# Optimization experiments

Measured on AMD Instinct MI355X. Metric: run time of the kernel, lower is better.

## Reference

```python
import jax, jax.numpy as jnp
import numpy as np
import math

SCALE = 35.0
MARGIN = 0.5
THRESH = -math.cos(MARGIN)          # easy_margin=False branch
SIN_M = math.sin(MARGIN)
OUT_INDICATOR = 1.0                 # easy_margin=False branch

B, D, C = 256, 128, 100000


def setup_inputs() -> dict:
    key = jax.random.key(0)
    k1, k2, k3 = jax.random.split(key, 3)
    feat = jax.random.normal(k1, (B, D), dtype=jnp.float32)
    # xavier_uniform over [class_num, feature_dim]
    limit = math.sqrt(6.0 / (C + D))
    weights = jax.random.uniform(k2, (C, D), dtype=jnp.float32, minval=-limit, maxval=limit)
    label = jax.random.randint(k3, (B,), 0, C, dtype=jnp.int64)
    return {"feat": feat, "weights": weights, "label": label}


def reference(feat, weights, label):
    # cosine similarity between l2-normalized features and class weights
    nf = feat / jnp.linalg.norm(feat, axis=-1, keepdims=True)          # [B, D]
    nw = weights / jnp.linalg.norm(weights, axis=-1, keepdims=True)    # [C, D]
    cos = jnp.einsum('bd,cd->bc', nf, nw)                              # [B, C]
    innerproduct_logits = jnp.einsum('bd,cd->bc', feat, weights)       # [B, C]

    rows = jnp.arange(cos.shape[0])
    cos_gt = cos[rows, label]                                          # [B]

    # margin tables are zero off the ground-truth column, so
    # cos(acos(cos)+0) == cos there: only the gt entry changes.
    cond = cos_gt > THRESH
    add_m = jnp.where(cond, MARGIN, 0.0)
    ext = jnp.where(cond, 0.0, -MARGIN * SIN_M) * OUT_INDICATOR
    # clip for acos numerical safety (matmul of normalized vecs can exceed 1 by eps)
    gt_marg = jnp.cos(jnp.arccos(jnp.clip(cos_gt, -1.0, 1.0)) + add_m) + ext

    marginal_logits = (SCALE * cos).at[rows, label].set(SCALE * gt_marg)
    return (cos, marginal_logits, innerproduct_logits)
```

## Files before the change

### kernel.cpp

```cpp
#include <hip/hip_runtime.h>
#include <math.h>

using short8  = __attribute__((ext_vector_type(8))) short;
using floatx4 = __attribute__((ext_vector_type(4))) float;

namespace {
constexpr int   kB      = 256;
constexpr int   kD      = 128;
constexpr int   kC      = 100000;
constexpr float kScale  = 35.0f;
constexpr float kCosM   = 0.87758256189037276f;
constexpr float kSinM   = 0.47942553860420301f;
constexpr float kThresh = -0.87758256189037276f;
constexpr float kExt    = -0.5f * 0.47942553860420301f;

constexpr size_t kFeatBfOff = 0;
constexpr size_t kRfOff     = (size_t)kB * 256;
}

__device__ inline unsigned short f2bf(float f) {
    unsigned u = __builtin_bit_cast(unsigned, f);
    return (unsigned short)((u + 0x7fffu + ((u >> 16) & 1u)) >> 16);
}

__device__ inline void async16(void* lds, const void* g) {
    __builtin_amdgcn_global_load_lds(
        (const __attribute__((address_space(1))) void*)g,
        (__attribute__((address_space(3))) void*)lds, 16, 0, 0);
}

__global__ __launch_bounds__(256)
void arcface_prep(const float* __restrict__ feat, unsigned char* __restrict__ ws) {
    const int wid = blockIdx.x * 4 + (threadIdx.x >> 6);
    const int l   = threadIdx.x & 63;
    const float2 v = *(const float2*)(feat + (size_t)wid * kD + 2 * l);
    float s = v.x * v.x + v.y * v.y;
    #pragma unroll
    for (int off = 32; off > 0; off >>= 1) s += __shfl_down(s, off, 64);
    const unsigned packed = (unsigned)f2bf(v.x) | ((unsigned)f2bf(v.y) << 16);
    ((unsigned*)(ws + kFeatBfOff + (size_t)wid * 256))[l] = packed;
    if (l == 0) *(float*)(ws + kRfOff + (size_t)wid * 4) = rsqrtf(s);
}

__global__ __launch_bounds__(256, 2)
void arcface_gemm(const float* __restrict__ wgt,
                  const unsigned char* __restrict__ ws,
                  float* __restrict__ out_cos,
                  float* __restrict__ out_marg,
                  float* __restrict__ out_ip) {
    __shared__ float sW[64 * 128];
    __shared__ float sScr[4][16 * 68];
    __shared__ float sRw[64];

    const int t   = threadIdx.x;
    const int l   = t & 63;
    const int w   = t >> 6;
    const int q   = l >> 4;
    const int c16 = l & 15;
    const int m0  = w * 64;
    const int c0  = blockIdx.x * 64;

    #pragma unroll
    for (int p = 0; p < 8; ++p) {
        const int o    = p * 4096 + t * 16;
        const int row  = o >> 9;
        const int col  = o & 511;
        const int swz  = ((row & 15) << 5) | ((row & 4) << 2);
        const int srow = min(c0 + row, kC - 1);
        async16((char*)sW + o, (const char*)wgt + (size_t)srow * 512 + (col ^ swz));
    }

    const short* featbf = (const short*)(ws + kFeatBfOff);
    const float* rf_g   = (const float*)(ws + kRfOff);

    short8 aF[4][4];
    #pragma unroll
    for (int mi = 0; mi < 4; ++mi)
        #pragma unroll
        for (int kq = 0; kq < 4; ++kq)
            aF[mi][kq] = *(const short8*)(featbf + (size_t)(m0 + mi * 16 + c16) * kD + kq * 32 + q * 8);

    __syncthreads();

    floatx4 acc[4][4];
    #pragma unroll
    for (int mi = 0; mi < 4; ++mi)
        #pragma unroll
        for (int nt = 0; nt < 4; ++nt)
            acc[mi][nt] = (floatx4){0.f, 0.f, 0.f, 0.f};

    float s2[4] = {0.f, 0.f, 0.f, 0.f};

    #pragma unroll
    for (int kq = 0; kq < 4; ++kq) {
        short8 bF[4];
        #pragma unroll
        for (int nt = 0; nt < 4; ++nt) {
            const int row = nt * 16 + c16;
            const int swz = ((row & 15) << 5) | ((row & 4) << 2);
            const int cb  = kq * 128 + q * 32;
            const floatx4 w0 = *(const floatx4*)((const char*)sW + row * 512 + ((cb)      ^ swz));
            const floatx4 w1 = *(const floatx4*)((const char*)sW + row * 512 + ((cb + 16) ^ swz));
            s2[nt] += w0[0]*w0[0] + w0[1]*w0[1] + w0[2]*w0[2] + w0[3]*w0[3]
                    + w1[0]*w1[0] + w1[1]*w1[1] + w1[2]*w1[2] + w1[3]*w1[3];
            short8 b;
            b[0] = (short)f2bf(w0[0]); b[1] = (short)f2bf(w0[1]);
            b[2] = (short)f2bf(w0[2]); b[3] = (short)f2bf(w0[3]);
            b[4] = (short)f2bf(w1[0]); b[5] = (short)f2bf(w1[1]);
            b[6] = (short)f2bf(w1[2]); b[7] = (short)f2bf(w1[3]);
            bF[nt] = b;
        }
        #pragma unroll
        for (int mi = 0; mi < 4; ++mi)
            #pragma unroll
            for (int nt = 0; nt < 4; ++nt)
                acc[mi][nt] = __builtin_amdgcn_mfma_f32_16x16x32_bf16(
                    aF[mi][kq], bF[nt], acc[mi][nt], 0, 0, 0);
    }

    #pragma unroll
    for (int nt = 0; nt < 4; ++nt) {
        float s = s2[nt];
        s += __shfl_xor(s, 16, 64);
        s += __shfl_xor(s, 32, 64);
        sRw[nt * 16 + c16] = rsqrtf(s);
    }

    float* scr = &sScr[w][0];
    const int  c   = c0 + c16 * 4;
    const bool cok = c < kC;
    const floatx4 rw4 = *(const floatx4*)(sRw + c16 * 4);

    #pragma unroll
    for (int mi = 0; mi < 4; ++mi) {
        #pragma unroll
        for (int nt = 0; nt < 4; ++nt)
            #pragma unroll
            for (int r = 0; r < 4; ++r)
                scr[(q * 4 + r) * 68 + nt * 16 + c16] = acc[mi][nt][r];
        #pragma unroll
        for (int jj = 0; jj < 4; ++jj) {
            const int rr = q + 4 * jj;
            const floatx4 ip = *(const floatx4*)(scr + rr * 68 + c16 * 4);
            const int m = m0 + mi * 16 + rr;
            if (cok) {
                const float rf = rf_g[m];
                const floatx4 cs = ip * rf * rw4;
                const size_t o = (size_t)m * kC + c;
                __builtin_nontemporal_store(ip,           (floatx4*)(out_ip + o));
                __builtin_nontemporal_store(cs,           (floatx4*)(out_cos + o));
                __builtin_nontemporal_store(cs * kScale,  (floatx4*)(out_marg + o));
            }
        }
    }
}

__global__ void arcface_fixup(const int* __restrict__ label,
                              const float* __restrict__ out_cos,
                              float* __restrict__ out_marg) {
    const int b = threadIdx.x;
    bool is64 = true;
    #pragma unroll
    for (int i = 1; i < 24; i += 2) is64 = is64 && (label[i] == 0);
    const int c = is64 ? label[2 * b] : label[b];
    const size_t idx = (size_t)b * kC + c;
    const float cosv = out_cos[idx];
    const float cc = fminf(1.f, fmaxf(-1.f, cosv));
    float marg;
    if (cosv > kThresh) {
        marg = cc * kCosM - sqrtf(fmaxf(0.f, 1.f - cc * cc)) * kSinM;
    } else {
        marg = cc + kExt;
    }
    out_marg[idx] = kScale * marg;
}

extern "C" void kernel_launch(void* const* d_in, const int* in_sizes, int n_in,
                              void* d_out, int out_size, void* d_ws, size_t ws_size,
                              hipStream_t stream) {
    const float* feat  = (const float*)d_in[0];
    const float* wgt   = (const float*)d_in[1];
    const int*   label = (const int*)d_in[2];
    float* out_cos  = (float*)d_out;
    float* out_marg = out_cos  + (size_t)kB * kC;
    float* out_ip   = out_marg + (size_t)kB * kC;
    unsigned char* ws = (unsigned char*)d_ws;

    arcface_prep<<<64, 256, 0, stream>>>(feat, ws);
    arcface_gemm<<<(kC + 63) / 64, 256, 0, stream>>>(wgt, ws, out_cos, out_marg, out_ip);
    arcface_fixup<<<1, 256, 0, stream>>>(label, out_cos, out_marg);
}
```

Measured before the change: 358.2 us.

## Switch GEMM to persistent per-wave tiles loading weights directly from global

```diff
diff --git a/kernel.cpp b/kernel.cpp
--- a/kernel.cpp
+++ b/kernel.cpp
@@ -16,17 +16,16 @@
 
 constexpr size_t kFeatBfOff = 0;
 constexpr size_t kRfOff     = (size_t)kB * 256;
+
+constexpr int kNgroups   = (kC + 63) / 64;
+constexpr int kTiles     = 8 * kNgroups;
+constexpr int kGemmGrid  = 512;
+constexpr int kWaveSlots = kGemmGrid * 4;
 }
 
 __device__ inline unsigned short f2bf(float f) {
     unsigned u = __builtin_bit_cast(unsigned, f);
     return (unsigned short)((u + 0x7fffu + ((u >> 16) & 1u)) >> 16);
-}
-
-__device__ inline void async16(void* lds, const void* g) {
-    __builtin_amdgcn_global_load_lds(
-        (const __attribute__((address_space(1))) void*)g,
-        (__attribute__((address_space(3))) void*)lds, 16, 0, 0);
 }
 
 __global__ __launch_bounds__(256)
@@ -48,108 +47,100 @@
                   float* __restrict__ out_cos,
                   float* __restrict__ out_marg,
                   float* __restrict__ out_ip) {
-    __shared__ float sW[64 * 128];
     __shared__ float sScr[4][16 * 68];
-    __shared__ float sRw[64];
+    __shared__ float sRw[4][64];
 
     const int t   = threadIdx.x;
     const int l   = t & 63;
     const int w   = t >> 6;
     const int q   = l >> 4;
     const int c16 = l & 15;
-    const int m0  = w * 64;
-    const int c0  = blockIdx.x * 64;
-
-    #pragma unroll
-    for (int p = 0; p < 8; ++p) {
-        const int o    = p * 4096 + t * 16;
-        const int row  = o >> 9;
-        const int col  = o & 511;
-        const int swz  = ((row & 15) << 5) | ((row & 4) << 2);
-        const int srow = min(c0 + row, kC - 1);
-        async16((char*)sW + o, (const char*)wgt + (size_t)srow * 512 + (col ^ swz));
-    }
 
     const short* featbf = (const short*)(ws + kFeatBfOff);
     const float* rf_g   = (const float*)(ws + kRfOff);
+    float* scr = &sScr[w][0];
+    float* rwp = &sRw[w][0];
 
-    short8 aF[4][4];
-    #pragma unroll
-    for (int mi = 0; mi < 4; ++mi)
+    for (int tile = blockIdx.x * 4 + w; tile < kTiles; tile += kWaveSlots) {
+        const int mg = tile & 7;
+        const int ng = tile >> 3;
+        const int m0 = mg * 32;
+        const int c0 = ng * 64;
+
+        short8 aF[2][4];
         #pragma unroll
-        for (int kq = 0; kq < 4; ++kq)
-            aF[mi][kq] = *(const short8*)(featbf + (size_t)(m0 + mi * 16 + c16) * kD + kq * 32 + q * 8);
+        for (int mi = 0; mi < 2; ++mi)
+            #pragma unroll
+            for (int kq = 0; kq < 4; ++kq)
+                aF[mi][kq] = *(const short8*)(featbf + (size_t)(m0 + mi * 16 + c16) * kD + kq * 32 + q * 8);
 
-    __syncthreads();
+        floatx4 acc[2][4];
+        #pragma unroll
+        for (int mi = 0; mi < 2; ++mi)
+            #pragma unroll
+            for (int nt = 0; nt < 4; ++nt)
+                acc[mi][nt] = (floatx4){0.f, 0.f, 0.f, 0.f};
 
-    floatx4 acc[4][4];
-    #pragma unroll
-    for (int mi = 0; mi < 4; ++mi)
+        float s2[4] = {0.f, 0.f, 0.f, 0.f};
+
         #pragma unroll
-        for (int nt = 0; nt < 4; ++nt)
-            acc[mi][nt] = (floatx4){0.f, 0.f, 0.f, 0.f};
+        for (int kq = 0; kq < 4; ++kq) {
+            short8 bF[4];
+            #pragma unroll
+            for (int nt = 0; nt < 4; ++nt) {
+                const int n = min(c0 + nt * 16 + c16, kC - 1);
+                const float* src = wgt + (size_t)n * kD + kq * 32 + q * 8;
+                const floatx4 w0 = *(const floatx4*)(src);
+                const floatx4 w1 = *(const floatx4*)(src + 4);
+                s2[nt] += w0[0]*w0[0] + w0[1]*w0[1] + w0[2]*w0[2] + w0[3]*w0[3]
+                        + w1[0]*w1[0] + w1[1]*w1[1] + w1[2]*w1[2] + w1[3]*w1[3];
+                short8 b;
+                b[0] = (short)f2bf(w0[0]); b[1] = (short)f2bf(w0[1]);
+                b[2] = (short)f2bf(w0[2]); b[3] = (short)f2bf(w0[3]);
+                b[4] = (short)f2bf(w1[0]); b[5] = (short)f2bf(w1[1]);
+                b[6] = (short)f2bf(w1[2]); b[7] = (short)f2bf(w1[3]);
+                bF[nt] = b;
+            }
+            #pragma unroll
+            for (int mi = 0; mi < 2; ++mi)
+                #pragma unroll
+                for (int nt = 0; nt < 4; ++nt)
+                    acc[mi][nt] = __builtin_amdgcn_mfma_f32_16x16x32_bf16(
+                        aF[mi][kq], bF[nt], acc[mi][nt], 0, 0, 0);
+        }
 
-    float s2[4] = {0.f, 0.f, 0.f, 0.f};
-
-    #pragma unroll
-    for (int kq = 0; kq < 4; ++kq) {
-        short8 bF[4];
         #pragma unroll
         for (int nt = 0; nt < 4; ++nt) {
-            const int row = nt * 16 + c16;
-            const int swz = ((row & 15) << 5) | ((row & 4) << 2);
-            const int cb  = kq * 128 + q * 32;
-            const floatx4 w0 = *(const floatx4*)((const char*)sW + row * 512 + ((cb)      ^ swz));
-            const floatx4 w1 = *(const floatx4*)((const char*)sW + row * 512 + ((cb + 16) ^ swz));
-            s2[nt] += w0[0]*w0[0] + w0[1]*w0[1] + w0[2]*w0[2] + w0[3]*w0[3]
-                    + w1[0]*w1[0] + w1[1]*w1[1] + w1[2]*w1[2] + w1[3]*w1[3];
-            short8 b;
-            b[0] = (short)f2bf(w0[0]); b[1] = (short)f2bf(w0[1]);
-            b[2] = (short)f2bf(w0[2]); b[3] = (short)f2bf(w0[3]);
-            b[4] = (short)f2bf(w1[0]); b[5] = (short)f2bf(w1[1]);
-            b[6] = (short)f2bf(w1[2]); b[7] = (short)f2bf(w1[3]);
-            bF[nt] = b;
+            float s = s2[nt];
+            s += __shfl_xor(s, 16, 64);
+            s += __shfl_xor(s, 32, 64);
+            rwp[nt * 16 + c16] = rsqrtf(s);
         }
+
+        const int  c   = c0 + c16 * 4;
+        const bool cok = c < kC;
+        const floatx4 rw4 = *(const floatx4*)(rwp + c16 * 4);
+
         #pragma unroll
-        for (int mi = 0; mi < 4; ++mi)
+        for (int mi = 0; mi < 2; ++mi) {
             #pragma unroll
             for (int nt = 0; nt < 4; ++nt)
-                acc[mi][nt] = __builtin_amdgcn_mfma_f32_16x16x32_bf16(
-                    aF[mi][kq], bF[nt], acc[mi][nt], 0, 0, 0);
-    }
-
-    #pragma unroll
-    for (int nt = 0; nt < 4; ++nt) {
-        float s = s2[nt];
-        s += __shfl_xor(s, 16, 64);
-        s += __shfl_xor(s, 32, 64);
-        sRw[nt * 16 + c16] = rsqrtf(s);
-    }
-
-    float* scr = &sScr[w][0];
-    const int  c   = c0 + c16 * 4;
-    const bool cok = c < kC;
-    const floatx4 rw4 = *(const floatx4*)(sRw + c16 * 4);
-
-    #pragma unroll
-    for (int mi = 0; mi < 4; ++mi) {
-        #pragma unroll
-        for (int nt = 0; nt < 4; ++nt)
+                #pragma unroll
+                for (int r = 0; r < 4; ++r)
+                    scr[(q * 4 + r) * 68 + nt * 16 + c16] = acc[mi][nt][r];
             #pragma unroll
-            for (int r = 0; r < 4; ++r)
-                scr[(q * 4 + r) * 68 + nt * 16 + c16] = acc[mi][nt][r];
-        #pragma unroll
-        for (int jj = 0; jj < 4; ++jj) {
-            const int rr = q + 4 * jj;
-            const floatx4 ip = *(const floatx4*)(scr + rr * 68 + c16 * 4);
-            const int m = m0 + mi * 16 + rr;
-            if (cok) {
-                const float rf = rf_g[m];
-                const floatx4 cs = ip * rf * rw4;
-                const size_t o = (size_t)m * kC + c;
-                __builtin_nontemporal_store(ip,           (floatx4*)(out_ip + o));
-                __builtin_nontemporal_store(cs,           (floatx4*)(out_cos + o));
-                __builtin_nontemporal_store(cs * kScale,  (floatx4*)(out_marg + o));
+            for (int jj = 0; jj < 4; ++jj) {
+                const int rr = q + 4 * jj;
+                const floatx4 ip = *(const floatx4*)(scr + rr * 68 + c16 * 4);
+                const int m = m0 + mi * 16 + rr;
+                if (cok) {
+                    const float rf = rf_g[m];
+                    const floatx4 cs = ip * rf * rw4;
+                    const size_t o = (size_t)m * kC + c;
+                    __builtin_nontemporal_store(ip,          (floatx4*)(out_ip + o));
+                    __builtin_nontemporal_store(cs,          (floatx4*)(out_cos + o));
+                    __builtin_nontemporal_store(cs * kScale, (floatx4*)(out_marg + o));
+                }
             }
         }
     }
@@ -187,6 +178,6 @@
     unsigned char* ws = (unsigned char*)d_ws;
 
     arcface_prep<<<64, 256, 0, stream>>>(feat, ws);
-    arcface_gemm<<<(kC + 63) / 64, 256, 0, stream>>>(wgt, ws, out_cos, out_marg, out_ip);
+    arcface_gemm<<<kGemmGrid, 256, 0, stream>>>(wgt, ws, out_cos, out_marg, out_ip);
     arcface_fixup<<<1, 256, 0, stream>>>(label, out_cos, out_marg);
 }
```

Result: slower. 389.2 us (+8.6%).
